# Performance work log

Hardware: AMD Instinct MI355X
Metric: run time of the kernel (lower is better)

Reference implementation:

```python
import jax, jax.numpy as jnp
import numpy as np

B, N, D, H, ND = 16, 512, 768, 12, 32
DK = D // H  # 64
GRID = 11    # hard-coded 11x11 patch grid in SpatialCirclePosition.patch


def setup_inputs() -> dict:
    key = jax.random.key(0)
    ks = jax.random.split(key, 10)
    features = jax.random.normal(ks[0], (B, N, D), dtype=jnp.float32)
    boxes = jax.random.uniform(ks[1], (B, N, 4), dtype=jnp.float32)  # normalized [0,1]
    sizes_wh = jax.random.randint(ks[2], (B, 2), 512, 1024).astype(jnp.int32)
    image_sizes = jnp.concatenate([sizes_wh, sizes_wh], axis=-1)  # (B,4) = [w,h,w,h]
    s = 0.02
    Wq = jax.random.normal(ks[3], (D, D), dtype=jnp.float32) * s
    Wk = jax.random.normal(ks[4], (D, D), dtype=jnp.float32) * s
    Wv = jax.random.normal(ks[5], (D, D), dtype=jnp.float32) * s
    Wo = jax.random.normal(ks[6], (D, D), dtype=jnp.float32) * s
    bq = jnp.zeros((D,), jnp.float32); bk = jnp.zeros((D,), jnp.float32)
    bv = jnp.zeros((D,), jnp.float32); bo = jnp.zeros((D,), jnp.float32)
    gamma = jnp.ones((D,), jnp.float32); beta = jnp.zeros((D,), jnp.float32)
    dist_emb = jax.random.normal(ks[7], (ND, H), dtype=jnp.float32) * s
    return {"features": features, "boxes": boxes, "image_sizes": image_sizes,
            "Wq": Wq, "bq": bq, "Wk": Wk, "bk": bk, "Wv": Wv, "bv": bv,
            "Wo": Wo, "bo": bo, "gamma": gamma, "beta": beta, "dist_emb": dist_emb}


def _patch_bins(boxes_norm, image_sizes):
    # boxes_norm: (B,N,4) in [0,1]; image_sizes: (B,4)=[w,h,w,h] int
    sizes_f = image_sizes.astype(jnp.float32)
    boxes = boxes_norm * sizes_f[:, None, :]                       # pixel boxes
    spa = jnp.floor_divide(sizes_f[:, :2], 11.0)                   # (B,2) size_per_area
    lb = jnp.arange(GRID, dtype=jnp.float32)                       # (11,)
    hb = lb + 1.0
    wlb = lb[None, :] * spa[:, 0:1]; whb = hb[None, :] * spa[:, 0:1]   # (B,11)
    hlb = lb[None, :] * spa[:, 1:2]; hhb = hb[None, :] * spa[:, 1:2]
    cx = jnp.floor_divide(boxes[..., 0] + boxes[..., 2], 2.0)      # (B,N)
    cy = jnp.floor_divide(boxes[..., 1] + boxes[..., 3], 2.0)
    mx = (wlb[:, None, :] <= cx[..., None]) & (cx[..., None] <= whb[:, None, :])  # (B,N,11)
    my = (hlb[:, None, :] <= cy[..., None]) & (cy[..., None] <= hhb[:, None, :])
    px = jnp.argmax(mx.astype(jnp.float32), axis=-1)               # (B,N) int
    py = jnp.argmax(my.astype(jnp.float32), axis=-1)
    return px.astype(jnp.float32), py.astype(jnp.float32)


def _dist_bins(boxes_norm, image_sizes):
    px, py = _patch_bins(boxes_norm, image_sizes)
    dx = px[:, None, :] - px[:, :, None]                           # (B,N,N)
    dy = py[:, None, :] - py[:, :, None]
    dist = jnp.sqrt(dx * dx + dy * dy) * 2.0
    return dist.astype(jnp.int32)                                  # truncation == .long()


def reference(features, boxes, image_sizes, Wq, bq, Wk, bk, Wv, bv, Wo, bo, gamma, beta, dist_emb):
    # LayerNorm(d_model), eps matches torch default 1e-5
    mu = jnp.mean(features, axis=-1, keepdims=True)
    var = jnp.mean(jnp.square(features - mu), axis=-1, keepdims=True)
    x = (features - mu) * jax.lax.rsqrt(var + 1e-5) * gamma + beta

    bins = _dist_bins(boxes, image_sizes)                          # (B,N,N) int32
    dist_bias = dist_emb[bins]                                     # (B,N,N,H)
    dist_bias = jnp.transpose(dist_bias, (0, 3, 1, 2))             # (B,H,N,N)

    bsz, nq, _ = x.shape
    q = (x @ Wq.T + bq).reshape(bsz, nq, H, DK).transpose(0, 2, 1, 3)  # (B,H,N,DK)
    k = (x @ Wk.T + bk).reshape(bsz, nq, H, DK).transpose(0, 2, 1, 3)
    v = (x @ Wv.T + bv).reshape(bsz, nq, H, DK).transpose(0, 2, 1, 3)

    att = jnp.einsum('bhqd,bhkd->bhqk', q, k) / np.sqrt(DK).astype(np.float32)
    att = jax.nn.softmax(att + dist_bias, axis=-1)                 # (B,H,N,N)
    out = jnp.einsum('bhqk,bhkd->bhqd', att, v)
    out = out.transpose(0, 2, 1, 3).reshape(bsz, nq, H * DK)
    out = out @ Wo.T + bo
    return out, att
```

## Files before the change

kernel.cpp:

```cpp
#include <hip/hip_runtime.h>
#include <hip/hip_bf16.h>

typedef unsigned char uchar;
typedef __attribute__((ext_vector_type(8))) short bf16x8;
typedef __attribute__((ext_vector_type(4))) float f32x4;

__device__ __forceinline__ unsigned short f2bf(float f) {
  union { float f; unsigned int u; } v; v.f = f;
  unsigned int u = v.u + 0x7fffu + ((v.u >> 16) & 1u);
  return (unsigned short)(u >> 16);
}

__device__ __forceinline__ void async_cp16(void* lds, const void* g) {
  __builtin_amdgcn_global_load_lds(
      (const __attribute__((address_space(1))) unsigned int*)g,
      (__attribute__((address_space(3))) unsigned int*)lds, 16, 0, 0);
}

__global__ void pxpy_kernel(const float* __restrict__ boxes, const int* __restrict__ isz,
                            float* __restrict__ px, float* __restrict__ py) {
  int idx = blockIdx.x * 256 + threadIdx.x;
  int b = idx >> 9;
  float w = (float)isz[b * 4 + 0];
  float h = (float)isz[b * 4 + 1];
  float b0 = boxes[idx * 4 + 0] * w;
  float b1 = boxes[idx * 4 + 1] * h;
  float b2 = boxes[idx * 4 + 2] * w;
  float b3 = boxes[idx * 4 + 3] * h;
  float spw = floorf(w / 11.0f);
  float sph = floorf(h / 11.0f);
  float cx = floorf((b0 + b2) * 0.5f);
  float cy = floorf((b1 + b3) * 0.5f);
  int pxi = 0, pyi = 0;
  bool fx = false, fy = false;
  for (int j = 0; j < 11; ++j) {
    float jf = (float)j;
    if (!fx && jf * spw <= cx && cx <= (jf + 1.0f) * spw) { pxi = j; fx = true; }
    if (!fy && jf * sph <= cy && cy <= (jf + 1.0f) * sph) { pyi = j; fy = true; }
  }
  px[idx] = (float)pxi;
  py[idx] = (float)pyi;
}

__global__ void bins_kernel(const float* __restrict__ px, const float* __restrict__ py,
                            uchar* __restrict__ bins) {
  int r = blockIdx.x;
  int j = threadIdx.x;
  int b = r >> 9;
  float pxq = px[r], pyq = py[r];
  float dx = px[b * 512 + j] - pxq;
  float dy = py[b * 512 + j] - pyq;
  float d = sqrtf(dx * dx + dy * dy) * 2.0f;
  bins[(size_t)r * 512 + j] = (uchar)(int)d;
}

__global__ __launch_bounds__(256) void ln_kernel(const float* __restrict__ f,
                                                 const float* __restrict__ gamma,
                                                 const float* __restrict__ beta,
                                                 unsigned short* __restrict__ x) {
  const int r = blockIdx.x;
  const int t = threadIdx.x;
  const float* row = f + (size_t)r * 768;
  float e0 = row[t], e1 = row[t + 256], e2 = row[t + 512];
  float s = e0 + e1 + e2;
#pragma unroll
  for (int off = 32; off > 0; off >>= 1) s += __shfl_down(s, off);
  __shared__ float red[4];
  const int wid = t >> 6;
  if ((t & 63) == 0) red[wid] = s;
  __syncthreads();
  float mean = (red[0] + red[1] + red[2] + red[3]) * (1.0f / 768.0f);
  __syncthreads();
  float d0 = e0 - mean, d1 = e1 - mean, d2 = e2 - mean;
  float v = d0 * d0 + d1 * d1 + d2 * d2;
#pragma unroll
  for (int off = 32; off > 0; off >>= 1) v += __shfl_down(v, off);
  if ((t & 63) == 0) red[wid] = v;
  __syncthreads();
  float var = (red[0] + red[1] + red[2] + red[3]) * (1.0f / 768.0f);
  float rs = rsqrtf(var + 1e-5f);
  x[(size_t)r * 768 + t]       = f2bf(d0 * rs * gamma[t] + beta[t]);
  x[(size_t)r * 768 + t + 256] = f2bf(d1 * rs * gamma[t + 256] + beta[t + 256]);
  x[(size_t)r * 768 + t + 512] = f2bf(d2 * rs * gamma[t + 512] + beta[t + 512]);
}

__global__ void wprep_kernel(const float* __restrict__ Wq, const float* __restrict__ Wk,
                             const float* __restrict__ Wv, const float* __restrict__ Wo,
                             const float* __restrict__ bq, const float* __restrict__ bk,
                             const float* __restrict__ bv,
                             unsigned short* __restrict__ wcat, unsigned short* __restrict__ wo,
                             float* __restrict__ bcat) {
  int idx = blockIdx.x * 256 + threadIdx.x;
  if (idx < 1769472) {
    int n = idx / 768, k = idx % 768;
    float v = (n < 768) ? Wq[n * 768 + k]
            : (n < 1536) ? Wk[(n - 768) * 768 + k]
                         : Wv[(n - 1536) * 768 + k];
    wcat[idx] = f2bf(v);
  } else {
    int j = idx - 1769472;
    wo[j] = f2bf(Wo[j]);
  }
  if (idx < 2304)
    bcat[idx] = (idx < 768) ? bq[idx] : (idx < 1536) ? bk[idx - 768] : bv[idx - 1536];
}

template <bool OUTF32>
__global__ __launch_bounds__(256) void gemm_bt(const unsigned short* __restrict__ A,
                                               const unsigned short* __restrict__ Bt,
                                               const float* __restrict__ bias,
                                               void* __restrict__ Cout, int K, int ldc) {
  __shared__ unsigned short a_lds[128 * 32];
  __shared__ unsigned short b_lds[128 * 32];
  const int m0 = blockIdx.x * 128, n0 = blockIdx.y * 128;
  const int tid = threadIdx.x;
  const int lane = tid & 63, wid = tid >> 6;
  const int ln = lane & 15, quad = lane >> 4;
  const int wm = (wid & 1) * 64, wn = (wid >> 1) * 64;
  f32x4 acc[16] = {};
  for (int k0 = 0; k0 < K; k0 += 32) {
    __syncthreads();
#pragma unroll
    for (int rep = 0; rep < 2; ++rep) {
      int c = rep * 256 + tid;
      int row = c >> 2, e0 = (c & 3) << 3;
      async_cp16(&a_lds[c * 8], A + (size_t)(m0 + row) * K + k0 + e0);
      async_cp16(&b_lds[c * 8], Bt + (size_t)(n0 + row) * K + k0 + e0);
    }
    __syncthreads();
    bf16x8 af[4], bfr[4];
#pragma unroll
    for (int i = 0; i < 4; ++i)
      af[i] = *(const bf16x8*)&a_lds[(wm + i * 16 + ln) * 32 + quad * 8];
#pragma unroll
    for (int j = 0; j < 4; ++j)
      bfr[j] = *(const bf16x8*)&b_lds[(wn + j * 16 + ln) * 32 + quad * 8];
#pragma unroll
    for (int i = 0; i < 4; ++i)
#pragma unroll
      for (int j = 0; j < 4; ++j)
        acc[i * 4 + j] = __builtin_amdgcn_mfma_f32_16x16x32_bf16(af[i], bfr[j], acc[i * 4 + j], 0, 0, 0);
  }
#pragma unroll
  for (int i = 0; i < 4; ++i)
#pragma unroll
    for (int j = 0; j < 4; ++j)
#pragma unroll
      for (int r = 0; r < 4; ++r) {
        int rr = m0 + wm + i * 16 + quad * 4 + r;
        int cc = n0 + wn + j * 16 + ln;
        float v = acc[i * 4 + j][r] + bias[cc];
        if (OUTF32) ((float*)Cout)[(size_t)rr * ldc + cc] = v;
        else ((unsigned short*)Cout)[(size_t)rr * ldc + cc] = f2bf(v);
      }
}

__global__ __launch_bounds__(256) void attn_fused(const unsigned short* __restrict__ qkv,
                                                  const uchar* __restrict__ bins,
                                                  const float* __restrict__ dist_emb,
                                                  float* __restrict__ att,
                                                  unsigned short* __restrict__ attnout) {
  const int bidx = blockIdx.x;
  const int qt = bidx & 7;
  const int h = (bidx >> 3) % 12;
  const int b = bidx / 96;
  __shared__ unsigned short qs[64 * 72];
  __shared__ unsigned short ks[64 * 72];
  __shared__ float demb[32];
  const int tid = threadIdx.x;
  if (tid < 32) demb[tid] = dist_emb[tid * 12 + h];
#pragma unroll
  for (int rep = 0; rep < 2; ++rep) {
    int c = rep * 256 + tid;
    int i = c >> 3, e0 = (c & 7) * 8;
    *(uint4*)&qs[i * 72 + e0] =
        *(const uint4*)(qkv + (size_t)(b * 512 + qt * 64 + i) * 2304 + h * 64 + e0);
  }
  const int lane = tid & 63, wid = tid >> 6;
  const int ln = lane & 15, quad = lane >> 4;
  f32x4 acc[32] = {};
  __syncthreads();
  bf16x8 a0 = *(const bf16x8*)&qs[(wid * 16 + ln) * 72 + quad * 8];
  bf16x8 a1 = *(const bf16x8*)&qs[(wid * 16 + ln) * 72 + 32 + quad * 8];
#pragma unroll
  for (int kc = 0; kc < 8; ++kc) {
    __syncthreads();
#pragma unroll
    for (int rep = 0; rep < 2; ++rep) {
      int c = rep * 256 + tid;
      int i = c >> 3, e0 = (c & 7) * 8;
      *(uint4*)&ks[i * 72 + e0] =
          *(const uint4*)(qkv + (size_t)(b * 512 + kc * 64 + i) * 2304 + 768 + h * 64 + e0);
    }
    __syncthreads();
#pragma unroll
    for (int t = 0; t < 4; ++t) {
      bf16x8 b0 = *(const bf16x8*)&ks[(t * 16 + ln) * 72 + quad * 8];
      bf16x8 b1 = *(const bf16x8*)&ks[(t * 16 + ln) * 72 + 32 + quad * 8];
      acc[kc * 4 + t] = __builtin_amdgcn_mfma_f32_16x16x32_bf16(a0, b0, acc[kc * 4 + t], 0, 0, 0);
      acc[kc * 4 + t] = __builtin_amdgcn_mfma_f32_16x16x32_bf16(a1, b1, acc[kc * 4 + t], 0, 0, 0);
    }
  }
  const int brow0 = qt * 64 + wid * 16 + quad * 4;
  const uchar* binb = bins + (size_t)b * 512 * 512;
#pragma unroll
  for (int i = 0; i < 32; ++i) {
    int col = (i >> 2) * 64 + (i & 3) * 16 + ln;
#pragma unroll
    for (int r = 0; r < 4; ++r) {
      int bin = binb[(size_t)(brow0 + r) * 512 + col];
      acc[i][r] = acc[i][r] * 0.125f + demb[bin];
    }
  }
  float inv[4];
#pragma unroll
  for (int r = 0; r < 4; ++r) {
    float m = -1e30f;
#pragma unroll
    for (int i = 0; i < 32; ++i) m = fmaxf(m, acc[i][r]);
    m = fmaxf(m, __shfl_xor(m, 1));
    m = fmaxf(m, __shfl_xor(m, 2));
    m = fmaxf(m, __shfl_xor(m, 4));
    m = fmaxf(m, __shfl_xor(m, 8));
    float s = 0.f;
#pragma unroll
    for (int i = 0; i < 32; ++i) { float p = __expf(acc[i][r] - m); acc[i][r] = p; s += p; }
    s += __shfl_xor(s, 1); s += __shfl_xor(s, 2); s += __shfl_xor(s, 4); s += __shfl_xor(s, 8);
    inv[r] = 1.0f / s;
  }
#pragma unroll
  for (int i = 0; i < 32; ++i)
#pragma unroll
    for (int r = 0; r < 4; ++r) acc[i][r] *= inv[(r)];
  float* ob = att + (size_t)((b * 12 + h) * 512) * 512;
#pragma unroll
  for (int i = 0; i < 32; ++i) {
    int col = (i >> 2) * 64 + (i & 3) * 16 + ln;
#pragma unroll
    for (int r = 0; r < 4; ++r)
      __builtin_nontemporal_store(acc[i][r], &ob[(size_t)(brow0 + r) * 512 + col]);
  }
  f32x4 acc_o[4] = {};
#pragma unroll
  for (int kc = 0; kc < 8; ++kc) {
    __syncthreads();
#pragma unroll
    for (int t = 0; t < 4; ++t)
#pragma unroll
      for (int r = 0; r < 4; ++r)
        qs[(wid * 16 + quad * 4 + r) * 72 + t * 16 + ln] = f2bf(acc[kc * 4 + t][r]);
#pragma unroll
    for (int rep = 0; rep < 2; ++rep) {
      int c = rep * 256 + tid;
      int n = c >> 3, e0 = (c & 7) * 8;
      uint4 xv = *(const uint4*)(qkv + (size_t)(b * 512 + kc * 64 + n) * 2304 + 1536 + h * 64 + e0);
      const unsigned short* xs = (const unsigned short*)&xv;
#pragma unroll
      for (int j = 0; j < 8; ++j) ks[(e0 + j) * 72 + n] = xs[j];
    }
    __syncthreads();
#pragma unroll
    for (int kk = 0; kk < 2; ++kk) {
      bf16x8 af = *(const bf16x8*)&qs[(wid * 16 + ln) * 72 + kk * 32 + quad * 8];
#pragma unroll
      for (int ct = 0; ct < 4; ++ct) {
        bf16x8 bg = *(const bf16x8*)&ks[(ct * 16 + ln) * 72 + kk * 32 + quad * 8];
        acc_o[ct] = __builtin_amdgcn_mfma_f32_16x16x32_bf16(af, bg, acc_o[ct], 0, 0, 0);
      }
    }
  }
#pragma unroll
  for (int ct = 0; ct < 4; ++ct)
#pragma unroll
    for (int r = 0; r < 4; ++r) {
      int m = b * 512 + qt * 64 + wid * 16 + quad * 4 + r;
      int cc = h * 64 + ct * 16 + ln;
      attnout[(size_t)m * 768 + cc] = f2bf(acc_o[ct][r]);
    }
}

extern "C" void kernel_launch(void* const* d_in, const int* in_sizes, int n_in,
                              void* d_out, int out_size, void* d_ws, size_t ws_size,
                              hipStream_t stream) {
  const float* features = (const float*)d_in[0];
  const float* boxes    = (const float*)d_in[1];
  const int*   isz      = (const int*)d_in[2];
  const float* Wq = (const float*)d_in[3];
  const float* bq = (const float*)d_in[4];
  const float* Wk = (const float*)d_in[5];
  const float* bk = (const float*)d_in[6];
  const float* Wv = (const float*)d_in[7];
  const float* bv = (const float*)d_in[8];
  const float* Wo = (const float*)d_in[9];
  const float* bo = (const float*)d_in[10];
  const float* gamma = (const float*)d_in[11];
  const float* beta  = (const float*)d_in[12];
  const float* dist_emb = (const float*)d_in[13];

  float* out = (float*)d_out;
  float* att = out + (size_t)8192 * 768;

  char* w = (char*)d_ws;
  float* px = (float*)w;          w += 8192 * 4;
  float* py = (float*)w;          w += 8192 * 4;
  uchar* bins = (uchar*)w;        w += (size_t)16 * 512 * 512;
  unsigned short* x = (unsigned short*)w;       w += (size_t)8192 * 768 * 2;
  unsigned short* wcat = (unsigned short*)w;    w += (size_t)2304 * 768 * 2;
  unsigned short* wo = (unsigned short*)w;      w += (size_t)768 * 768 * 2;
  float* bcat = (float*)w;                      w += 2304 * 4;
  unsigned short* qkv = (unsigned short*)w;     w += (size_t)8192 * 2304 * 2;
  unsigned short* attnout = (unsigned short*)w; w += (size_t)8192 * 768 * 2;

  pxpy_kernel<<<32, 256, 0, stream>>>(boxes, isz, px, py);
  bins_kernel<<<8192, 512, 0, stream>>>(px, py, bins);
  ln_kernel<<<8192, 256, 0, stream>>>(features, gamma, beta, x);
  wprep_kernel<<<9216, 256, 0, stream>>>(Wq, Wk, Wv, Wo, bq, bk, bv, wcat, wo, bcat);
  gemm_bt<false><<<dim3(64, 18), 256, 0, stream>>>(x, wcat, bcat, qkv, 768, 2304);
  attn_fused<<<1536, 256, 0, stream>>>(qkv, bins, dist_emb, att, attnout);
  gemm_bt<true><<<dim3(64, 6), 256, 0, stream>>>(attnout, wo, bo, out, 768, 768);
}
```

Before: 452.8 us.

## Double-buffer K/V tiles with register prefetch and swizzle V/P LDS layouts

The fused attention kernel now keeps two LDS buffers for K and V. It prefetches the next 64-row chunk into registers while MFMAs run on the current chunk, which cuts one barrier per iteration. The transposed V tile and the bf16 probability tile use an XOR swizzle to reduce LDS bank conflicts. The fp32 attention-matrix stores are spread across the PV loop as ordinary stores instead of one nontemporal burst, and s_setprio is raised around the MFMA blocks. This costs extra registers and LDS, which may lower occupancy.

Result: faster. 442.2 us (-2.3%).

```diff
diff --git a/kernel.cpp b/kernel.cpp
--- a/kernel.cpp
+++ b/kernel.cpp
@@ -165,42 +165,57 @@
   const int h = (bidx >> 3) % 12;
   const int b = bidx / 96;
   __shared__ unsigned short qs[64 * 72];
-  __shared__ unsigned short ks[64 * 72];
+  __shared__ unsigned short ks[2][64 * 72];
   __shared__ float demb[32];
   const int tid = threadIdx.x;
-  if (tid < 32) demb[tid] = dist_emb[tid * 12 + h];
-#pragma unroll
-  for (int rep = 0; rep < 2; ++rep) {
-    int c = rep * 256 + tid;
-    int i = c >> 3, e0 = (c & 7) * 8;
-    *(uint4*)&qs[i * 72 + e0] =
-        *(const uint4*)(qkv + (size_t)(b * 512 + qt * 64 + i) * 2304 + h * 64 + e0);
-  }
   const int lane = tid & 63, wid = tid >> 6;
   const int ln = lane & 15, quad = lane >> 4;
-  f32x4 acc[32] = {};
+  if (tid < 32) demb[tid] = dist_emb[tid * 12 + h];
+
+  {
+    int i0 = tid >> 3, e0 = (tid & 7) * 8;
+    *(uint4*)&qs[i0 * 72 + e0] =
+        *(const uint4*)(qkv + (size_t)(b * 512 + qt * 64 + i0) * 2304 + h * 64 + e0);
+    *(uint4*)&qs[(i0 + 32) * 72 + e0] =
+        *(const uint4*)(qkv + (size_t)(b * 512 + qt * 64 + i0 + 32) * 2304 + h * 64 + e0);
+  }
+  const int si = tid >> 3, se = (tid & 7) * 8;
+  const unsigned short* kbase = qkv + (size_t)(b * 512) * 2304 + 768 + h * 64 + se;
+  const unsigned short* vbase = qkv + (size_t)(b * 512) * 2304 + 1536 + h * 64 + se;
+  uint4 kr0 = *(const uint4*)(kbase + (size_t)si * 2304);
+  uint4 kr1 = *(const uint4*)(kbase + (size_t)(si + 32) * 2304);
   __syncthreads();
   bf16x8 a0 = *(const bf16x8*)&qs[(wid * 16 + ln) * 72 + quad * 8];
   bf16x8 a1 = *(const bf16x8*)&qs[(wid * 16 + ln) * 72 + 32 + quad * 8];
-#pragma unroll
+  *(uint4*)&ks[0][si * 72 + se] = kr0;
+  *(uint4*)&ks[0][(si + 32) * 72 + se] = kr1;
+  __syncthreads();
+  f32x4 acc[32] = {};
   for (int kc = 0; kc < 8; ++kc) {
-    __syncthreads();
-#pragma unroll
-    for (int rep = 0; rep < 2; ++rep) {
-      int c = rep * 256 + tid;
-      int i = c >> 3, e0 = (c & 7) * 8;
-      *(uint4*)&ks[i * 72 + e0] =
-          *(const uint4*)(qkv + (size_t)(b * 512 + kc * 64 + i) * 2304 + 768 + h * 64 + e0);
-    }
-    __syncthreads();
+    const unsigned short* cur = ks[kc & 1];
+    if (kc < 7) {
+      kr0 = *(const uint4*)(kbase + (size_t)((kc + 1) * 64 + si) * 2304);
+      kr1 = *(const uint4*)(kbase + (size_t)((kc + 1) * 64 + si + 32) * 2304);
+    }
+    __builtin_amdgcn_s_setprio(1);
 #pragma unroll
     for (int t = 0; t < 4; ++t) {
-      bf16x8 b0 = *(const bf16x8*)&ks[(t * 16 + ln) * 72 + quad * 8];
-      bf16x8 b1 = *(const bf16x8*)&ks[(t * 16 + ln) * 72 + 32 + quad * 8];
+      bf16x8 b0 = *(const bf16x8*)&cur[(t * 16 + ln) * 72 + quad * 8];
+      bf16x8 b1 = *(const bf16x8*)&cur[(t * 16 + ln) * 72 + 32 + quad * 8];
       acc[kc * 4 + t] = __builtin_amdgcn_mfma_f32_16x16x32_bf16(a0, b0, acc[kc * 4 + t], 0, 0, 0);
       acc[kc * 4 + t] = __builtin_amdgcn_mfma_f32_16x16x32_bf16(a1, b1, acc[kc * 4 + t], 0, 0, 0);
     }
-  }
+    __builtin_amdgcn_s_setprio(0);
+    if (kc < 7) {
+      unsigned short* nxt = ks[(kc + 1) & 1];
+      *(uint4*)&nxt[si * 72 + se] = kr0;
+      *(uint4*)&nxt[(si + 32) * 72 + se] = kr1;
+      __syncthreads();
+    }
+  }
+  uint4 vr0 = *(const uint4*)(vbase + (size_t)si * 2304);
+  uint4 vr1 = *(const uint4*)(vbase + (size_t)(si + 32) * 2304);
+
   const int brow0 = qt * 64 + wid * 16 + quad * 4;
   const uchar* binb = bins + (size_t)b * 512 * 512;
 #pragma unroll
@@ -231,42 +246,74 @@
 #pragma unroll
   for (int i = 0; i < 32; ++i)
 #pragma unroll
-    for (int r = 0; r < 4; ++r) acc[i][r] *= inv[(r)];
+    for (int r = 0; r < 4; ++r) acc[i][r] *= inv[r];
+
+  {
+    const unsigned short* xs = (const unsigned short*)&vr0;
+#pragma unroll
+    for (int j = 0; j < 8; ++j) {
+      int d = se + j;
+      ks[0][d * 72 + (si ^ (((d >> 3) & 7) << 3))] = xs[j];
+    }
+    xs = (const unsigned short*)&vr1;
+#pragma unroll
+    for (int j = 0; j < 8; ++j) {
+      int d = se + j;
+      ks[0][d * 72 + ((si + 32) ^ (((d >> 3) & 7) << 3))] = xs[j];
+    }
+  }
+  __syncthreads();
+  f32x4 acc_o[4] = {};
   float* ob = att + (size_t)((b * 12 + h) * 512) * 512;
-#pragma unroll
-  for (int i = 0; i < 32; ++i) {
-    int col = (i >> 2) * 64 + (i & 3) * 16 + ln;
-#pragma unroll
-    for (int r = 0; r < 4; ++r)
-      __builtin_nontemporal_store(acc[i][r], &ob[(size_t)(brow0 + r) * 512 + col]);
-  }
-  f32x4 acc_o[4] = {};
-#pragma unroll
   for (int kc = 0; kc < 8; ++kc) {
-    __syncthreads();
+    const unsigned short* cur = ks[kc & 1];
+    if (kc < 7) {
+      vr0 = *(const uint4*)(vbase + (size_t)((kc + 1) * 64 + si) * 2304);
+      vr1 = *(const uint4*)(vbase + (size_t)((kc + 1) * 64 + si + 32) * 2304);
+    }
 #pragma unroll
     for (int t = 0; t < 4; ++t)
 #pragma unroll
+      for (int r = 0; r < 4; ++r) {
+        int row = wid * 16 + quad * 4 + r;
+        int col = (t * 16 + ln) ^ (((row >> 2) & 7) << 3);
+        qs[row * 72 + col] = f2bf(acc[kc * 4 + t][r]);
+      }
+    __builtin_amdgcn_s_setprio(1);
+#pragma unroll
+    for (int kk = 0; kk < 2; ++kk) {
+      int prow = wid * 16 + ln;
+      int pcol = (kk * 32 + quad * 8) ^ (((prow >> 2) & 7) << 3);
+      bf16x8 af = *(const bf16x8*)&qs[prow * 72 + pcol];
+#pragma unroll
+      for (int ct = 0; ct < 4; ++ct) {
+        int d = ct * 16 + ln;
+        int vcol = (kk * 32 + quad * 8) ^ (((d >> 3) & 7) << 3);
+        bf16x8 bg = *(const bf16x8*)&cur[d * 72 + vcol];
+        acc_o[ct] = __builtin_amdgcn_mfma_f32_16x16x32_bf16(af, bg, acc_o[ct], 0, 0, 0);
+      }
+    }
+    __builtin_amdgcn_s_setprio(0);
+#pragma unroll
+    for (int t = 0; t < 4; ++t)
+#pragma unroll
       for (int r = 0; r < 4; ++r)
-        qs[(wid * 16 + quad * 4 + r) * 72 + t * 16 + ln] = f2bf(acc[kc * 4 + t][r]);
-#pragma unroll
-    for (int rep = 0; rep < 2; ++rep) {
-      int c = rep * 256 + tid;
-      int n = c >> 3, e0 = (c & 7) * 8;
-      uint4 xv = *(const uint4*)(qkv + (size_t)(b * 512 + kc * 64 + n) * 2304 + 1536 + h * 64 + e0);
-      const unsigned short* xs = (const unsigned short*)&xv;
-#pragma unroll
-      for (int j = 0; j < 8; ++j) ks[(e0 + j) * 72 + n] = xs[j];
-    }
-    __syncthreads();
-#pragma unroll
-    for (int kk = 0; kk < 2; ++kk) {
-      bf16x8 af = *(const bf16x8*)&qs[(wid * 16 + ln) * 72 + kk * 32 + quad * 8];
-#pragma unroll
-      for (int ct = 0; ct < 4; ++ct) {
-        bf16x8 bg = *(const bf16x8*)&ks[(ct * 16 + ln) * 72 + kk * 32 + quad * 8];
-        acc_o[ct] = __builtin_amdgcn_mfma_f32_16x16x32_bf16(af, bg, acc_o[ct], 0, 0, 0);
-      }
+        ob[(size_t)(brow0 + r) * 512 + kc * 64 + t * 16 + ln] = acc[kc * 4 + t][r];
+    if (kc < 7) {
+      unsigned short* nxt = ks[(kc + 1) & 1];
+      const unsigned short* xs = (const unsigned short*)&vr0;
+#pragma unroll
+      for (int j = 0; j < 8; ++j) {
+        int d = se + j;
+        nxt[d * 72 + (si ^ (((d >> 3) & 7) << 3))] = xs[j];
+      }
+      xs = (const unsigned short*)&vr1;
+#pragma unroll
+      for (int j = 0; j < 8; ++j) {
+        int d = se + j;
+        nxt[d * 72 + ((si + 32) ^ (((d >> 3) & 7) << 3))] = xs[j];
+      }
+      __syncthreads();
     }
   }
 #pragma unroll
```
